# Performance work log

Hardware: AMD Instinct MI355X
Metric: run time of the kernel (lower is better)

Reference implementation:

```python
import jax, jax.numpy as jnp
import numpy as np

EMBED_DIM = 256
NUM_HEADS = 8
HEAD_DIM = EMBED_DIM // NUM_HEADS
SCALE = HEAD_DIM ** -0.5  # note: scale uses head_dim even though attention is over full D
EPS = 1e-12  # torch F.normalize eps


def setup_inputs() -> dict:
    key = jax.random.key(0)
    k1, k2, k3 = jax.random.split(key, 3)
    B, Nq, Nk, D = 4, 4096, 4096, EMBED_DIM
    return {
        "query": jax.random.normal(k1, (B, Nq, D), dtype=jnp.float32),
        "key": jax.random.normal(k2, (B, Nk, D), dtype=jnp.float32),
        "value": jax.random.normal(k3, (B, Nk, D), dtype=jnp.float32),
    }


def _l2_normalize(x):
    # matches torch.nn.functional.normalize(x, dim=-1): x / max(||x||, eps)
    n = jnp.linalg.norm(x, axis=-1, keepdims=True)
    return x / jnp.maximum(n, EPS)


def reference(query, key, value):
    q = _l2_normalize(query)          # (B, Nq, D)
    k = _l2_normalize(key)            # (B, Nk, D)
    scores = jnp.einsum("bqd,bkd->bqk", q, k) * SCALE  # (B, Nq, Nk) cosine sims
    attn = jax.nn.softmax(scores, axis=-1)
    return jnp.einsum("bqk,bkd->bqd", attn, value)     # (B, Nq, D)
```

## Files before the change

kernel.cpp:

```cpp
#include <hip/hip_runtime.h>


#define NQ 4096
#define DIM 256
#define NROWS 16384
#define BM 64
#define BN 64
#define KSPLIT 2
#define NITER 32
#define PSTRIDE 68

typedef __attribute__((ext_vector_type(8))) short bf16x8;
typedef __attribute__((ext_vector_type(4))) float f32x4;
typedef __attribute__((ext_vector_type(16))) float f32x16;

__device__ __forceinline__ unsigned short f2bf(float f) {
  unsigned int u = __float_as_uint(f);
  u += 0x7fffu + ((u >> 16) & 1u);
  return (unsigned short)(u >> 16);
}

__device__ __forceinline__ float bf2f(unsigned short h) {
  return __uint_as_float((unsigned int)h << 16);
}

__device__ __forceinline__ unsigned int pack2bf(float a, float b) {
  unsigned int ua = __float_as_uint(a) + 0x8000u;
  unsigned int ub = __float_as_uint(b) + 0x8000u;
  return __builtin_amdgcn_perm(ub, ua, 0x07060302u);
}

__device__ __forceinline__ void gload16(const void* g, void* l) {
  __builtin_amdgcn_global_load_lds(
      (const __attribute__((address_space(1))) unsigned int*)g,
      (__attribute__((address_space(3))) unsigned int*)l, 16, 0, 0);
}

__global__ __launch_bounds__(256) void prep(
    const float* __restrict__ K, const float* __restrict__ V,
    unsigned short* __restrict__ Kfm, unsigned short* __restrict__ Vfm)
{
  __shared__ unsigned short vt[32 * 264];
  const int blk = blockIdx.x, tid = threadIdx.x;
  const int wave = tid >> 6, lane = tid & 63;
  if (blk < 512) {
    const int kt2 = blk;
    const int kt = kt2 >> 1, h = kt2 & 1;
    #pragma unroll
    for (int i = 0; i < 8; i++) {
      const int r = wave*8 + i;
      float4 v = *(const float4*)(K + ((size_t)kt2*32 + r) * DIM + lane * 4);
      float ss = v.x*v.x + v.y*v.y + v.z*v.z + v.w*v.w;
      #pragma unroll
      for (int off = 1; off < 64; off <<= 1) ss += __shfl_xor(ss, off, 64);
      float scale = 1.0f / fmaxf(sqrtf(ss), 1e-12f);
      ushort4 o;
      o.x = f2bf(v.x*scale); o.y = f2bf(v.y*scale);
      o.z = f2bf(v.z*scale); o.w = f2bf(v.w*scale);
      *(ushort4*)(vt + r*264 + lane*4) = o;
    }
    __syncthreads();
    #pragma unroll
    for (int s = 0; s < 4; s++) {
      const int ch = tid + 256*s;
      const int c = ch >> 5, r = ch & 31;
      const int n = h*32 + r;
      bf16x8 val = *(const bf16x8*)(vt + r*264 + c*8);
      *(bf16x8*)(Kfm + (size_t)kt*16384 + (size_t)(c*64 + n)*8) = val;
    }
  } else {
    const int NS = blk - 512;
    #pragma unroll
    for (int i = 0; i < 4; i++) {
      const int e = tid + 256*i;
      const int nl = e >> 6, d = (e & 63) * 4;
      float4 v = *(const float4*)(V + ((size_t)NS*16 + nl)*DIM + d);
      ushort4 o;
      o.x = f2bf(v.x); o.y = f2bf(v.y); o.z = f2bf(v.z); o.w = f2bf(v.w);
      *(ushort4*)(vt + nl*264 + d) = o;
    }
    __syncthreads();
    #pragma unroll
    for (int i = 0; i < 2; i++) {
      const int ch = tid + 256*i;
      const int db = ch >> 6, ln = ch & 63;
      const int row0 = (ln >> 5) * 8, dd = db*32 + (ln & 31);
      ushort4 a, b;
      a.x = vt[(row0+0)*264 + dd]; a.y = vt[(row0+1)*264 + dd];
      a.z = vt[(row0+2)*264 + dd]; a.w = vt[(row0+3)*264 + dd];
      b.x = vt[(row0+4)*264 + dd]; b.y = vt[(row0+5)*264 + dd];
      b.z = vt[(row0+6)*264 + dd]; b.w = vt[(row0+7)*264 + dd];
      size_t base = ((size_t)(NS*8 + db)*64 + ln)*8;
      *(ushort4*)(Vfm + base)     = a;
      *(ushort4*)(Vfm + base + 4) = b;
    }
  }
}

__global__ __launch_bounds__(256, 2) void attn(
    const float* __restrict__ Qg,
    const unsigned short* __restrict__ Kfm,
    const unsigned short* __restrict__ Vfm,
    unsigned short* __restrict__ Opart, float* __restrict__ lpart)
{
  __shared__ unsigned short Klds[32 * 64 * 8];
  __shared__ unsigned short Plds[BM * PSTRIDE];

  const int tid = threadIdx.x, wave = tid >> 6, lane = tid & 63;
  const int l15 = lane & 15, l4 = lane >> 4;
  const int blk = blockIdx.x;
  const int g = blk & 7, qt = blk >> 3;
  const int b = g >> 1, ks = g & 1;
  const int Rq0 = b*NQ + qt*BM;
  const int n0base = b*NQ + ks*(NQ/KSPLIT);
  const int mi = wave & 1, ni = wave >> 1;

  {
    unsigned short* Qlds = Klds;
    #pragma unroll
    for (int i = 0; i < 16; i++) {
      const int r = wave*16 + i;
      float4 v = *(const float4*)(Qg + (size_t)(Rq0 + r)*DIM + lane*4);
      float ss = v.x*v.x + v.y*v.y + v.z*v.z + v.w*v.w;
      #pragma unroll
      for (int off = 1; off < 64; off <<= 1) ss += __shfl_xor(ss, off, 64);
      float scale = (0.17677669529663687f * 1.4426950408889634f)
                    / fmaxf(sqrtf(ss), 1e-12f);
      ushort4 o;
      o.x = f2bf(v.x*scale); o.y = f2bf(v.y*scale);
      o.z = f2bf(v.z*scale); o.w = f2bf(v.w*scale);
      *(ushort4*)(Qlds + r*DIM + lane*4) = o;
    }
  }
  __syncthreads();

  bf16x8 qf[2][8];
  #pragma unroll
  for (int mt = 0; mt < 2; mt++) {
    const unsigned short* qrow = Klds + (mi*32 + mt*16 + l15)*DIM + l4*8;
    #pragma unroll
    for (int kg = 0; kg < 8; kg++)
      qf[mt][kg] = *(const bf16x8*)(qrow + kg*32);
  }
  __syncthreads();

  f32x16 oacc[2][2] = {};
  float lacc[2] = {};

  auto stage = [&](int kt) {
    const unsigned short* src = Kfm + (size_t)((n0base + kt*BN) >> 6) * (32*64*8);
    #pragma unroll
    for (int jj = 0; jj < 4; jj++) {
      const int c = wave*8 + jj*2;
      gload16(src + (size_t)c*512 + lane*8,     Klds + (size_t)c*512);
      gload16(src + (size_t)(c+1)*512 + lane*8, Klds + (size_t)(c+1)*512);
    }
  };

  stage(0);

  for (int kt = 0; kt < NITER; kt++) {
    __syncthreads();

    f32x4 sacc[2][2] = {};
    #pragma unroll
    for (int kg = 0; kg < 8; kg++) {
      bf16x8 kf[2];
      #pragma unroll
      for (int nt = 0; nt < 2; nt++) {
        const int nrow = ni*32 + nt*16 + l15;
        const int c = kg*4 + l4;
        kf[nt] = *(const bf16x8*)(Klds + ((size_t)(c*64 + nrow))*8);
      }
      #pragma unroll
      for (int nt = 0; nt < 2; nt++)
        #pragma unroll
        for (int mt = 0; mt < 2; mt++)
          sacc[nt][mt] = __builtin_amdgcn_mfma_f32_16x16x32_bf16(
              kf[nt], qf[mt][kg], sacc[nt][mt], 0, 0, 0);
    }

    #pragma unroll
    for (int nt = 0; nt < 2; nt++)
      #pragma unroll
      for (int mt = 0; mt < 2; mt++) {
        float p0 = __builtin_amdgcn_exp2f(sacc[nt][mt][0]);
        float p1 = __builtin_amdgcn_exp2f(sacc[nt][mt][1]);
        float p2 = __builtin_amdgcn_exp2f(sacc[nt][mt][2]);
        float p3 = __builtin_amdgcn_exp2f(sacc[nt][mt][3]);
        lacc[mt] += (p0 + p1) + (p2 + p3);
        uint2 pk;
        pk.x = pack2bf(p0, p1);
        pk.y = pack2bf(p2, p3);
        const int m = mi*32 + mt*16 + l15;
        const int n = ni*32 + nt*16 + 4*l4;
        *(uint2*)(Plds + m*PSTRIDE + n) = pk;
      }

    __syncthreads();

    if (kt + 1 < NITER) stage(kt + 1);

    const int NB0 = (n0base + kt*BN) >> 4;
    #pragma unroll
    for (int kstep = 0; kstep < 4; kstep++) {
      bf16x8 pf[2], vf[2];
      #pragma unroll
      for (int mt2 = 0; mt2 < 2; mt2++)
        pf[mt2] = *(const bf16x8*)(Plds + (mt2*32 + (lane & 31))*PSTRIDE
                                   + kstep*16 + 8*(lane >> 5));
      #pragma unroll
      for (int dt = 0; dt < 2; dt++) {
        const int db = wave*2 + dt;
        vf[dt] = *(const bf16x8*)(Vfm + ((size_t)((NB0 + kstep)*8 + db)*64 + lane)*8);
      }
      #pragma unroll
      for (int mt2 = 0; mt2 < 2; mt2++)
        #pragma unroll
        for (int dt = 0; dt < 2; dt++)
          oacc[mt2][dt] = __builtin_amdgcn_mfma_f32_32x32x16_bf16(
              pf[mt2], vf[dt], oacc[mt2][dt], 0, 0, 0);
    }
  }

  #pragma unroll
  for (int mt = 0; mt < 2; mt++) {
    float s = lacc[mt];
    s += __shfl_xor(s, 16, 64);
    s += __shfl_xor(s, 32, 64);
    if (l4 == 0)
      lpart[(size_t)(ks*2 + ni)*NROWS + Rq0 + mi*32 + mt*16 + l15] = s;
  }

  #pragma unroll
  for (int mt2 = 0; mt2 < 2; mt2++)
    #pragma unroll
    for (int dt = 0; dt < 2; dt++)
      #pragma unroll
      for (int reg = 0; reg < 16; reg++) {
        const int m = mt2*32 + 4*(lane >> 5) + (reg & 3) + 8*(reg >> 2);
        const int d = wave*64 + dt*32 + (lane & 31);
        Opart[((size_t)(ks*NROWS + Rq0 + m))*DIM + d] = f2bf(oacc[mt2][dt][reg]);
      }
}

__global__ __launch_bounds__(256) void combine(
    const unsigned short* __restrict__ Opart, const float* __restrict__ lpart,
    float* __restrict__ out)
{
  const size_t idx = (size_t)blockIdx.x*256 + threadIdx.x;
  const size_t e = idx*4;
  const int R = (int)(e >> 8);
  ushort4 o0 = *(const ushort4*)(Opart + e);
  ushort4 o1 = *(const ushort4*)(Opart + (size_t)NROWS*DIM + e);
  float ls = lpart[R] + lpart[NROWS + R] + lpart[2*NROWS + R] + lpart[3*NROWS + R];
  float inv = 1.0f / ls;
  float4 o;
  o.x = (bf2f(o0.x) + bf2f(o1.x))*inv;
  o.y = (bf2f(o0.y) + bf2f(o1.y))*inv;
  o.z = (bf2f(o0.z) + bf2f(o1.z))*inv;
  o.w = (bf2f(o0.w) + bf2f(o1.w))*inv;
  *(float4*)(out + e) = o;
}

extern "C" void kernel_launch(void* const* d_in, const int* in_sizes, int n_in,
                              void* d_out, int out_size, void* d_ws, size_t ws_size,
                              hipStream_t stream) {
  const float* Q = (const float*)d_in[0];
  const float* K = (const float*)d_in[1];
  const float* V = (const float*)d_in[2];
  char* ws = (char*)d_ws;
  unsigned short* Kfm   = (unsigned short*)(ws);
  unsigned short* Vfm   = (unsigned short*)(ws + 8388608);
  unsigned short* Opart = (unsigned short*)(ws + 16777216);
  float* lpart = (float*)(ws + 33554432);

  prep<<<1536, 256, 0, stream>>>(K, V, Kfm, Vfm);
  attn<<<512, 256, 0, stream>>>(Q, Kfm, Vfm, Opart, lpart);
  combine<<<4096, 256, 0, stream>>>(Opart, lpart, (float*)d_out);
}
```

Before: 174.6 us.

## Double-buffer K tiles in LDS and software-pipeline P/V fragment loads

K tiles now live in two LDS buffers. The next tile's async copy is issued at the top of each iteration, so it overlaps the QK^T and PV work instead of sitting between them. The barrier after writing P waits only on LDS counters, and P/V fragments are prefetched one k-step ahead into double-buffered registers. MFMA sections are wrapped in s_setprio. The costs are double the K LDS footprint, which may pressure occupancy at 2 blocks per CU, and more live registers. The in-order vmcnt may also make V loads wait behind the K prefetch.

```diff
diff --git a/kernel.cpp b/kernel.cpp
--- a/kernel.cpp
+++ b/kernel.cpp
@@ -103,7 +103,7 @@
     const unsigned short* __restrict__ Vfm,
     unsigned short* __restrict__ Opart, float* __restrict__ lpart)
 {
-  __shared__ unsigned short Klds[32 * 64 * 8];
+  __shared__ unsigned short Klds[2][32 * 64 * 8];
   __shared__ unsigned short Plds[BM * PSTRIDE];
 
   const int tid = threadIdx.x, wave = tid >> 6, lane = tid & 63;
@@ -116,7 +116,7 @@
   const int mi = wave & 1, ni = wave >> 1;
 
   {
-    unsigned short* Qlds = Klds;
+    unsigned short* Qlds = &Klds[0][0];
     #pragma unroll
     for (int i = 0; i < 16; i++) {
       const int r = wave*16 + i;
@@ -137,7 +137,7 @@
   bf16x8 qf[2][8];
   #pragma unroll
   for (int mt = 0; mt < 2; mt++) {
-    const unsigned short* qrow = Klds + (mi*32 + mt*16 + l15)*DIM + l4*8;
+    const unsigned short* qrow = &Klds[0][0] + (mi*32 + mt*16 + l15)*DIM + l4*8;
     #pragma unroll
     for (int kg = 0; kg < 8; kg++)
       qf[mt][kg] = *(const bf16x8*)(qrow + kg*32);
@@ -147,13 +147,14 @@
   f32x16 oacc[2][2] = {};
   float lacc[2] = {};
 
-  auto stage = [&](int kt) {
-    const unsigned short* src = Kfm + (size_t)((n0base + kt*BN) >> 6) * (32*64*8);
+  auto stage = [&](int kt_) {
+    unsigned short* dst = &Klds[kt_ & 1][0];
+    const unsigned short* src = Kfm + (size_t)((n0base + kt_*BN) >> 6) * (32*64*8);
     #pragma unroll
     for (int jj = 0; jj < 4; jj++) {
       const int c = wave*8 + jj*2;
-      gload16(src + (size_t)c*512 + lane*8,     Klds + (size_t)c*512);
-      gload16(src + (size_t)(c+1)*512 + lane*8, Klds + (size_t)(c+1)*512);
+      gload16(src + (size_t)c*512 + lane*8,     dst + (size_t)c*512);
+      gload16(src + (size_t)(c+1)*512 + lane*8, dst + (size_t)(c+1)*512);
     }
   };
 
@@ -161,6 +162,11 @@
 
   for (int kt = 0; kt < NITER; kt++) {
     __syncthreads();
+
+    if (kt + 1 < NITER) stage(kt + 1);
+    __builtin_amdgcn_sched_barrier(0);
+
+    const unsigned short* kb = &Klds[kt & 1][0];
 
     f32x4 sacc[2][2] = {};
     #pragma unroll
@@ -170,14 +176,16 @@
       for (int nt = 0; nt < 2; nt++) {
         const int nrow = ni*32 + nt*16 + l15;
         const int c = kg*4 + l4;
-        kf[nt] = *(const bf16x8*)(Klds + ((size_t)(c*64 + nrow))*8);
+        kf[nt] = *(const bf16x8*)(kb + ((size_t)(c*64 + nrow))*8);
       }
+      __builtin_amdgcn_s_setprio(1);
       #pragma unroll
       for (int nt = 0; nt < 2; nt++)
         #pragma unroll
         for (int mt = 0; mt < 2; mt++)
           sacc[nt][mt] = __builtin_amdgcn_mfma_f32_16x16x32_bf16(
               kf[nt], qf[mt][kg], sacc[nt][mt], 0, 0, 0);
+      __builtin_amdgcn_s_setprio(0);
     }
 
     #pragma unroll
@@ -197,29 +205,40 @@
         *(uint2*)(Plds + m*PSTRIDE + n) = pk;
       }
 
-    __syncthreads();
-
-    if (kt + 1 < NITER) stage(kt + 1);
+    asm volatile("s_waitcnt lgkmcnt(0)" ::: "memory");
+    __builtin_amdgcn_s_barrier();
+    __builtin_amdgcn_sched_barrier(0);
 
     const int NB0 = (n0base + kt*BN) >> 4;
+    bf16x8 pf[2][2], vf[2][2];
+    #pragma unroll
+    for (int mt2 = 0; mt2 < 2; mt2++)
+      pf[0][mt2] = *(const bf16x8*)(Plds + (mt2*32 + (lane & 31))*PSTRIDE
+                                    + 8*(lane >> 5));
+    #pragma unroll
+    for (int dt = 0; dt < 2; dt++)
+      vf[0][dt] = *(const bf16x8*)(Vfm + ((size_t)(NB0*8 + wave*2 + dt)*64 + lane)*8);
     #pragma unroll
     for (int kstep = 0; kstep < 4; kstep++) {
-      bf16x8 pf[2], vf[2];
-      #pragma unroll
-      for (int mt2 = 0; mt2 < 2; mt2++)
-        pf[mt2] = *(const bf16x8*)(Plds + (mt2*32 + (lane & 31))*PSTRIDE
-                                   + kstep*16 + 8*(lane >> 5));
-      #pragma unroll
-      for (int dt = 0; dt < 2; dt++) {
-        const int db = wave*2 + dt;
-        vf[dt] = *(const bf16x8*)(Vfm + ((size_t)((NB0 + kstep)*8 + db)*64 + lane)*8);
+      const int cb = kstep & 1;
+      if (kstep < 3) {
+        #pragma unroll
+        for (int mt2 = 0; mt2 < 2; mt2++)
+          pf[cb^1][mt2] = *(const bf16x8*)(Plds + (mt2*32 + (lane & 31))*PSTRIDE
+                                           + (kstep+1)*16 + 8*(lane >> 5));
+        #pragma unroll
+        for (int dt = 0; dt < 2; dt++)
+          vf[cb^1][dt] = *(const bf16x8*)(Vfm
+              + ((size_t)((NB0 + kstep + 1)*8 + wave*2 + dt)*64 + lane)*8);
       }
+      __builtin_amdgcn_s_setprio(1);
       #pragma unroll
       for (int mt2 = 0; mt2 < 2; mt2++)
         #pragma unroll
         for (int dt = 0; dt < 2; dt++)
           oacc[mt2][dt] = __builtin_amdgcn_mfma_f32_32x32x16_bf16(
-              pf[mt2], vf[dt], oacc[mt2][dt], 0, 0, 0);
+              pf[cb][mt2], vf[cb][dt], oacc[mt2][dt], 0, 0, 0);
+      __builtin_amdgcn_s_setprio(0);
     }
   }
 
```

New measurement: 173.9 us. Within noise of the previous version (-0.4%).

## Raise key split to four, add MFMA priority hints, allow three blocks per CU

Applied to the files above, without the earlier changes.

Templates the attention and combine kernels on the key-split factor and launches a 4-way split (1024 blocks) when the workspace is large enough, falling back to the old 2-way split otherwise. The goal is more blocks in flight to fill the CUs, with launch bounds raised to allow three blocks per CU. It also reorders the QK loop to load one K fragment at a time and wraps the MFMA groups in s_setprio to favour matrix issue. In exchange, the combine kernel reads twice the partial outputs, register pressure rises under the tighter launch bound, and the path depends on the workspace size.

```diff
diff --git a/kernel.cpp b/kernel.cpp
--- a/kernel.cpp
+++ b/kernel.cpp
@@ -6,8 +6,6 @@
 #define NROWS 16384
 #define BM 64
 #define BN 64
-#define KSPLIT 2
-#define NITER 32
 #define PSTRIDE 68
 
 typedef __attribute__((ext_vector_type(8))) short bf16x8;
@@ -97,22 +95,24 @@
   }
 }
 
-__global__ __launch_bounds__(256, 2) void attn(
+template<int KS>
+__global__ __launch_bounds__(256, 3) void attn(
     const float* __restrict__ Qg,
     const unsigned short* __restrict__ Kfm,
     const unsigned short* __restrict__ Vfm,
     unsigned short* __restrict__ Opart, float* __restrict__ lpart)
 {
+  constexpr int NITER = (NQ / KS) / BN;
   __shared__ unsigned short Klds[32 * 64 * 8];
   __shared__ unsigned short Plds[BM * PSTRIDE];
 
   const int tid = threadIdx.x, wave = tid >> 6, lane = tid & 63;
   const int l15 = lane & 15, l4 = lane >> 4;
   const int blk = blockIdx.x;
-  const int g = blk & 7, qt = blk >> 3;
-  const int b = g >> 1, ks = g & 1;
+  const int g = blk & (4*KS - 1), qt = blk / (4*KS);
+  const int b = g / KS, ks = g & (KS - 1);
   const int Rq0 = b*NQ + qt*BM;
-  const int n0base = b*NQ + ks*(NQ/KSPLIT);
+  const int n0base = b*NQ + ks*(NQ/KS);
   const int mi = wave & 1, ni = wave >> 1;
 
   {
@@ -147,8 +147,8 @@
   f32x16 oacc[2][2] = {};
   float lacc[2] = {};
 
-  auto stage = [&](int kt) {
-    const unsigned short* src = Kfm + (size_t)((n0base + kt*BN) >> 6) * (32*64*8);
+  auto stage = [&](int kt_) {
+    const unsigned short* src = Kfm + (size_t)((n0base + kt_*BN) >> 6) * (32*64*8);
     #pragma unroll
     for (int jj = 0; jj < 4; jj++) {
       const int c = wave*8 + jj*2;
@@ -164,20 +164,19 @@
 
     f32x4 sacc[2][2] = {};
     #pragma unroll
-    for (int kg = 0; kg < 8; kg++) {
-      bf16x8 kf[2];
-      #pragma unroll
-      for (int nt = 0; nt < 2; nt++) {
-        const int nrow = ni*32 + nt*16 + l15;
+    for (int nt = 0; nt < 2; nt++) {
+      const int nrow = ni*32 + nt*16 + l15;
+      #pragma unroll
+      for (int kg = 0; kg < 8; kg++) {
         const int c = kg*4 + l4;
-        kf[nt] = *(const bf16x8*)(Klds + ((size_t)(c*64 + nrow))*8);
-      }
-      #pragma unroll
-      for (int nt = 0; nt < 2; nt++)
+        bf16x8 kf = *(const bf16x8*)(Klds + ((size_t)(c*64 + nrow))*8);
+        __builtin_amdgcn_s_setprio(1);
         #pragma unroll
         for (int mt = 0; mt < 2; mt++)
           sacc[nt][mt] = __builtin_amdgcn_mfma_f32_16x16x32_bf16(
-              kf[nt], qf[mt][kg], sacc[nt][mt], 0, 0, 0);
+              kf, qf[mt][kg], sacc[nt][mt], 0, 0, 0);
+        __builtin_amdgcn_s_setprio(0);
+      }
     }
 
     #pragma unroll
@@ -214,12 +213,14 @@
         const int db = wave*2 + dt;
         vf[dt] = *(const bf16x8*)(Vfm + ((size_t)((NB0 + kstep)*8 + db)*64 + lane)*8);
       }
+      __builtin_amdgcn_s_setprio(1);
       #pragma unroll
       for (int mt2 = 0; mt2 < 2; mt2++)
         #pragma unroll
         for (int dt = 0; dt < 2; dt++)
           oacc[mt2][dt] = __builtin_amdgcn_mfma_f32_32x32x16_bf16(
               pf[mt2], vf[dt], oacc[mt2][dt], 0, 0, 0);
+      __builtin_amdgcn_s_setprio(0);
     }
   }
 
@@ -244,6 +245,7 @@
       }
 }
 
+template<int KS>
 __global__ __launch_bounds__(256) void combine(
     const unsigned short* __restrict__ Opart, const float* __restrict__ lpart,
     float* __restrict__ out)
@@ -251,15 +253,18 @@
   const size_t idx = (size_t)blockIdx.x*256 + threadIdx.x;
   const size_t e = idx*4;
   const int R = (int)(e >> 8);
-  ushort4 o0 = *(const ushort4*)(Opart + e);
-  ushort4 o1 = *(const ushort4*)(Opart + (size_t)NROWS*DIM + e);
-  float ls = lpart[R] + lpart[NROWS + R] + lpart[2*NROWS + R] + lpart[3*NROWS + R];
+  float ls = 0.0f;
+  #pragma unroll
+  for (int i = 0; i < 2*KS; i++) ls += lpart[(size_t)i*NROWS + R];
   float inv = 1.0f / ls;
-  float4 o;
-  o.x = (bf2f(o0.x) + bf2f(o1.x))*inv;
-  o.y = (bf2f(o0.y) + bf2f(o1.y))*inv;
-  o.z = (bf2f(o0.z) + bf2f(o1.z))*inv;
-  o.w = (bf2f(o0.w) + bf2f(o1.w))*inv;
+  float4 o = {0.0f, 0.0f, 0.0f, 0.0f};
+  #pragma unroll
+  for (int s = 0; s < KS; s++) {
+    ushort4 op = *(const ushort4*)(Opart + (size_t)s*NROWS*DIM + e);
+    o.x += bf2f(op.x); o.y += bf2f(op.y);
+    o.z += bf2f(op.z); o.w += bf2f(op.w);
+  }
+  o.x *= inv; o.y *= inv; o.z *= inv; o.w *= inv;
   *(float4*)(out + e) = o;
 }
 
@@ -273,9 +278,17 @@
   unsigned short* Kfm   = (unsigned short*)(ws);
   unsigned short* Vfm   = (unsigned short*)(ws + 8388608);
   unsigned short* Opart = (unsigned short*)(ws + 16777216);
-  float* lpart = (float*)(ws + 33554432);
 
   prep<<<1536, 256, 0, stream>>>(K, V, Kfm, Vfm);
-  attn<<<512, 256, 0, stream>>>(Q, Kfm, Vfm, Opart, lpart);
-  combine<<<4096, 256, 0, stream>>>(Opart, lpart, (float*)d_out);
-}
+
+  const size_t need4 = 16777216ull + 4ull*NROWS*DIM*2 + 8ull*NROWS*4;
+  if (ws_size >= need4) {
+    float* lpart = (float*)(ws + 16777216 + 4ull*NROWS*DIM*2);
+    attn<4><<<1024, 256, 0, stream>>>(Q, Kfm, Vfm, Opart, lpart);
+    combine<4><<<4096, 256, 0, stream>>>(Opart, lpart, (float*)d_out);
+  } else {
+    float* lpart = (float*)(ws + 16777216 + 2ull*NROWS*DIM*2);
+    attn<2><<<512, 256, 0, stream>>>(Q, Kfm, Vfm, Opart, lpart);
+    combine<2><<<4096, 256, 0, stream>>>(Opart, lpart, (float*)d_out);
+  }
+}
```

Result: slower. 205.6 us (+17.7%).

## Load K fragments directly from global, double-buffer P, single barrier per iteration

Applied to the files above, without the earlier changes.

Removes the LDS staging of K tiles (global_load_lds) and instead has each wave read its K MFMA fragments straight from the pre-swizzled global buffer, which should be L2-resident and shared across waves. P is double-buffered in LDS so only one barrier per iteration is needed instead of two. All V fragments for the tile are hoisted ahead of the softmax, and s_setprio wraps the MFMA blocks. This removes the LDS write/read traffic and one sync, but increases redundant global/L2 reads of K (each ni pair of waves loads the same rows) and register pressure from holding eight V fragments.

```diff
diff --git a/kernel.cpp b/kernel.cpp
--- a/kernel.cpp
+++ b/kernel.cpp
@@ -9,6 +9,7 @@
 #define KSPLIT 2
 #define NITER 32
 #define PSTRIDE 68
+#define PBUF (BM*PSTRIDE)
 
 typedef __attribute__((ext_vector_type(8))) short bf16x8;
 typedef __attribute__((ext_vector_type(4))) float f32x4;
@@ -28,12 +29,6 @@
   unsigned int ua = __float_as_uint(a) + 0x8000u;
   unsigned int ub = __float_as_uint(b) + 0x8000u;
   return __builtin_amdgcn_perm(ub, ua, 0x07060302u);
-}
-
-__device__ __forceinline__ void gload16(const void* g, void* l) {
-  __builtin_amdgcn_global_load_lds(
-      (const __attribute__((address_space(1))) unsigned int*)g,
-      (__attribute__((address_space(3))) unsigned int*)l, 16, 0, 0);
 }
 
 __global__ __launch_bounds__(256) void prep(
@@ -103,8 +98,7 @@
     const unsigned short* __restrict__ Vfm,
     unsigned short* __restrict__ Opart, float* __restrict__ lpart)
 {
-  __shared__ unsigned short Klds[32 * 64 * 8];
-  __shared__ unsigned short Plds[BM * PSTRIDE];
+  __shared__ unsigned short SH[64 * 256];
 
   const int tid = threadIdx.x, wave = tid >> 6, lane = tid & 63;
   const int l15 = lane & 15, l4 = lane >> 4;
@@ -115,29 +109,26 @@
   const int n0base = b*NQ + ks*(NQ/KSPLIT);
   const int mi = wave & 1, ni = wave >> 1;
 
-  {
-    unsigned short* Qlds = Klds;
-    #pragma unroll
-    for (int i = 0; i < 16; i++) {
-      const int r = wave*16 + i;
-      float4 v = *(const float4*)(Qg + (size_t)(Rq0 + r)*DIM + lane*4);
-      float ss = v.x*v.x + v.y*v.y + v.z*v.z + v.w*v.w;
-      #pragma unroll
-      for (int off = 1; off < 64; off <<= 1) ss += __shfl_xor(ss, off, 64);
-      float scale = (0.17677669529663687f * 1.4426950408889634f)
-                    / fmaxf(sqrtf(ss), 1e-12f);
-      ushort4 o;
-      o.x = f2bf(v.x*scale); o.y = f2bf(v.y*scale);
-      o.z = f2bf(v.z*scale); o.w = f2bf(v.w*scale);
-      *(ushort4*)(Qlds + r*DIM + lane*4) = o;
-    }
+  #pragma unroll
+  for (int i = 0; i < 16; i++) {
+    const int r = wave*16 + i;
+    float4 v = *(const float4*)(Qg + (size_t)(Rq0 + r)*DIM + lane*4);
+    float ss = v.x*v.x + v.y*v.y + v.z*v.z + v.w*v.w;
+    #pragma unroll
+    for (int off = 1; off < 64; off <<= 1) ss += __shfl_xor(ss, off, 64);
+    float scale = (0.17677669529663687f * 1.4426950408889634f)
+                  / fmaxf(sqrtf(ss), 1e-12f);
+    ushort4 o;
+    o.x = f2bf(v.x*scale); o.y = f2bf(v.y*scale);
+    o.z = f2bf(v.z*scale); o.w = f2bf(v.w*scale);
+    *(ushort4*)(SH + r*DIM + lane*4) = o;
   }
   __syncthreads();
 
   bf16x8 qf[2][8];
   #pragma unroll
   for (int mt = 0; mt < 2; mt++) {
-    const unsigned short* qrow = Klds + (mi*32 + mt*16 + l15)*DIM + l4*8;
+    const unsigned short* qrow = SH + (mi*32 + mt*16 + l15)*DIM + l4*8;
     #pragma unroll
     for (int kg = 0; kg < 8; kg++)
       qf[mt][kg] = *(const bf16x8*)(qrow + kg*32);
@@ -147,39 +138,38 @@
   f32x16 oacc[2][2] = {};
   float lacc[2] = {};
 
-  auto stage = [&](int kt) {
-    const unsigned short* src = Kfm + (size_t)((n0base + kt*BN) >> 6) * (32*64*8);
-    #pragma unroll
-    for (int jj = 0; jj < 4; jj++) {
-      const int c = wave*8 + jj*2;
-      gload16(src + (size_t)c*512 + lane*8,     Klds + (size_t)c*512);
-      gload16(src + (size_t)(c+1)*512 + lane*8, Klds + (size_t)(c+1)*512);
-    }
-  };
-
-  stage(0);
+  const unsigned short* Kt = Kfm + (size_t)(n0base >> 6) * 16384
+                             + ((size_t)l4*64 + ni*32 + l15)*8;
 
   for (int kt = 0; kt < NITER; kt++) {
-    __syncthreads();
-
     f32x4 sacc[2][2] = {};
     #pragma unroll
     for (int kg = 0; kg < 8; kg++) {
       bf16x8 kf[2];
       #pragma unroll
-      for (int nt = 0; nt < 2; nt++) {
-        const int nrow = ni*32 + nt*16 + l15;
-        const int c = kg*4 + l4;
-        kf[nt] = *(const bf16x8*)(Klds + ((size_t)(c*64 + nrow))*8);
-      }
+      for (int nt = 0; nt < 2; nt++)
+        kf[nt] = *(const bf16x8*)(Kt + (size_t)kg*2048 + nt*128);
+      __builtin_amdgcn_s_setprio(1);
       #pragma unroll
       for (int nt = 0; nt < 2; nt++)
         #pragma unroll
         for (int mt = 0; mt < 2; mt++)
           sacc[nt][mt] = __builtin_amdgcn_mfma_f32_16x16x32_bf16(
               kf[nt], qf[mt][kg], sacc[nt][mt], 0, 0, 0);
-    }
-
+      __builtin_amdgcn_s_setprio(0);
+    }
+    Kt += 16384;
+
+    const int NB0 = (n0base + kt*BN) >> 4;
+    bf16x8 vf[4][2];
+    #pragma unroll
+    for (int kstep = 0; kstep < 4; kstep++)
+      #pragma unroll
+      for (int dt = 0; dt < 2; dt++)
+        vf[kstep][dt] = *(const bf16x8*)(Vfm
+            + ((size_t)((NB0 + kstep)*8 + wave*2 + dt)*64 + lane)*8);
+
+    unsigned short* pb = SH + (kt & 1)*PBUF;
     #pragma unroll
     for (int nt = 0; nt < 2; nt++)
       #pragma unroll
@@ -194,32 +184,28 @@
         pk.y = pack2bf(p2, p3);
         const int m = mi*32 + mt*16 + l15;
         const int n = ni*32 + nt*16 + 4*l4;
-        *(uint2*)(Plds + m*PSTRIDE + n) = pk;
+        *(uint2*)(pb + m*PSTRIDE + n) = pk;
       }
 
-    __syncthreads();
-
-    if (kt + 1 < NITER) stage(kt + 1);
-
-    const int NB0 = (n0base + kt*BN) >> 4;
+    asm volatile("s_waitcnt lgkmcnt(0)" ::: "memory");
+    __builtin_amdgcn_s_barrier();
+    __builtin_amdgcn_sched_barrier(0);
+
     #pragma unroll
     for (int kstep = 0; kstep < 4; kstep++) {
-      bf16x8 pf[2], vf[2];
+      bf16x8 pf[2];
       #pragma unroll
       for (int mt2 = 0; mt2 < 2; mt2++)
-        pf[mt2] = *(const bf16x8*)(Plds + (mt2*32 + (lane & 31))*PSTRIDE
+        pf[mt2] = *(const bf16x8*)(pb + (mt2*32 + (lane & 31))*PSTRIDE
                                    + kstep*16 + 8*(lane >> 5));
-      #pragma unroll
-      for (int dt = 0; dt < 2; dt++) {
-        const int db = wave*2 + dt;
-        vf[dt] = *(const bf16x8*)(Vfm + ((size_t)((NB0 + kstep)*8 + db)*64 + lane)*8);
-      }
+      __builtin_amdgcn_s_setprio(1);
       #pragma unroll
       for (int mt2 = 0; mt2 < 2; mt2++)
         #pragma unroll
         for (int dt = 0; dt < 2; dt++)
           oacc[mt2][dt] = __builtin_amdgcn_mfma_f32_32x32x16_bf16(
-              pf[mt2], vf[dt], oacc[mt2][dt], 0, 0, 0);
+              pf[mt2], vf[kstep][dt], oacc[mt2][dt], 0, 0, 0);
+      __builtin_amdgcn_s_setprio(0);
     }
   }
 
```

Result: slower. 211.0 us (+20.8%).
